# Kernel optimization log

Hardware: AMD Instinct MI355X
Metric: run time of the kernel (lower is better)

The kernel has to match this reference:

```python
import jax, jax.numpy as jnp
import numpy as np

B, IN_DIM, D, P = 256, 1024, 512, 2048


def setup_inputs() -> dict:
    key = jax.random.key(0)
    ks = jax.random.split(key, 7)
    return {
        "x": jax.random.normal(ks[0], (B, IN_DIM), dtype=jnp.float32),
        "y": jax.random.randint(ks[1], (B,), 0, P),
        "Wb": jax.random.normal(ks[2], (D, IN_DIM), dtype=jnp.float32) * 0.02,
        "bb": jax.random.normal(ks[3], (D,), dtype=jnp.float32) * 0.02,
        "Wm": jax.random.normal(ks[4], (P, D), dtype=jnp.float32) * 0.02,
        "bm": jax.random.normal(ks[5], (P,), dtype=jnp.float32) * 0.02,
        "proxies": jax.random.normal(ks[6], (P, D), dtype=jnp.float32),
    }


def reference(x, y, Wb, bb, Wm, bm, proxies):
    # backbone: Linear(in_dim -> D)
    feat = x @ Wb.T + bb                         # [B, D]
    # L2-norm regularizer: mean of per-row L2 norms
    reg_e = jnp.mean(jnp.sqrt(jnp.sum(feat * feat, axis=1)))
    # multi: classification head Linear(D -> P)
    out = feat @ Wm.T + bm                       # [B, P]
    # squared euclidean distance to each proxy (broadcast diff + square + sum)
    den = jnp.sum((feat[:, None, :] - proxies[None, :, :]) ** 2, axis=2)  # [B, P]
    # cross-entropy on negated distances
    logp = jax.nn.log_softmax(-den, axis=1)      # [B, P]
    loss = -jnp.mean(jnp.take_along_axis(logp, y[:, None], axis=1))
    return out, loss, reg_e
```

## Files before the change

### kernel.cpp

```cpp
#include <hip/hip_runtime.h>
#include <hip/hip_bf16.h>
#include <math.h>

#define NB   256
#define KIN  1024
#define ND   512
#define NP   2048
#define NTOT 4096

typedef __bf16 bf16x8 __attribute__((ext_vector_type(8)));
typedef float  f32x4  __attribute__((ext_vector_type(4)));
typedef unsigned short ush8 __attribute__((ext_vector_type(8)));

#define OFF_WPB    0u
#define OFF_FEATB  4194304u
#define OFF_PN2    4456448u
#define OFF_LOGITS 4464640u
#define OFF_ROWLP  6561792u
#define OFF_ROWNM  6562816u

__device__ __forceinline__ float bf2f(unsigned short h) {
    union { unsigned u; float f; } v; v.u = ((unsigned)h) << 16; return v.f;
}

__device__ __forceinline__ ush8 pack8(float4 f0, float4 f1) {
    union { ush8 v; __hip_bfloat162 h[4]; } o;
    o.h[0] = __float22bfloat162_rn(make_float2(f0.x, f0.y));
    o.h[1] = __float22bfloat162_rn(make_float2(f0.z, f0.w));
    o.h[2] = __float22bfloat162_rn(make_float2(f1.x, f1.y));
    o.h[3] = __float22bfloat162_rn(make_float2(f1.z, f1.w));
    return o.v;
}

__global__ __launch_bounds__(256) void k_prep(
    const float* __restrict__ Wm, const float* __restrict__ prox,
    unsigned short* __restrict__ WPb, float* __restrict__ pn2)
{
    const int t = threadIdx.x, lane = t & 63, w = t >> 6;
    const int r = blockIdx.x * 4 + w;
    const float* src = (r < NP) ? (Wm + (size_t)r * ND)
                                : (prox + (size_t)(r - NP) * ND);
    float4 v0 = *(const float4*)(src + lane * 8);
    float4 v1 = *(const float4*)(src + lane * 8 + 4);
    *(ush8*)(WPb + (size_t)r * ND + lane * 8) = pack8(v0, v1);
    if (r >= NP) {
        float s = v0.x*v0.x + v0.y*v0.y + v0.z*v0.z + v0.w*v0.w
                + v1.x*v1.x + v1.y*v1.y + v1.z*v1.z + v1.w*v1.w;
#pragma unroll
        for (int off = 32; off; off >>= 1) s += __shfl_down(s, off);
        if (lane == 0) pn2[r - NP] = s;
    }
}

__global__ __launch_bounds__(256) void k_feat(
    const float* __restrict__ x, const float* __restrict__ Wb,
    const float* __restrict__ bb, unsigned short* __restrict__ featb)
{
    __shared__ unsigned short As[2][64 * 32];
    __shared__ unsigned short Bs[2][64 * 32];
    const int t = threadIdx.x, lane = t & 63, w = t >> 6;
    const int n0 = blockIdx.x * 64, m0 = blockIdx.y * 64;
    const int srow = t >> 2, sc = (t & 3) * 8;
    const float* gA = x  + (size_t)(m0 + srow) * KIN + sc;
    const float* gB = Wb + (size_t)(n0 + srow) * KIN + sc;
    float4 a0 = *(const float4*)gA, a1 = *(const float4*)(gA + 4);
    float4 b0 = *(const float4*)gB, b1 = *(const float4*)(gB + 4);
    f32x4 acc[2][2] = {};
    const int wm = (w >> 1) * 32, wn = (w & 1) * 32;
    const int arow = wm + (lane & 15), brow = wn + (lane & 15);
    const int fcol = (lane >> 4) * 8;
    for (int ks = 0; ks < KIN / 32; ++ks) {
        *(ush8*)&As[ks & 1][srow * 32 + sc] = pack8(a0, a1);
        *(ush8*)&Bs[ks & 1][srow * 32 + sc] = pack8(b0, b1);
        __syncthreads();
        if (ks + 1 < KIN / 32) {
            a0 = *(const float4*)(gA + (ks + 1) * 32);
            a1 = *(const float4*)(gA + (ks + 1) * 32 + 4);
            b0 = *(const float4*)(gB + (ks + 1) * 32);
            b1 = *(const float4*)(gB + (ks + 1) * 32 + 4);
        }
        const unsigned short* as = &As[ks & 1][0];
        const unsigned short* bs = &Bs[ks & 1][0];
        bf16x8 af0 = *(const bf16x8*)&as[(arow     ) * 32 + fcol];
        bf16x8 af1 = *(const bf16x8*)&as[(arow + 16) * 32 + fcol];
        bf16x8 bf0 = *(const bf16x8*)&bs[(brow     ) * 32 + fcol];
        bf16x8 bf1 = *(const bf16x8*)&bs[(brow + 16) * 32 + fcol];
        acc[0][0] = __builtin_amdgcn_mfma_f32_16x16x32_bf16(af0, bf0, acc[0][0], 0, 0, 0);
        acc[0][1] = __builtin_amdgcn_mfma_f32_16x16x32_bf16(af0, bf1, acc[0][1], 0, 0, 0);
        acc[1][0] = __builtin_amdgcn_mfma_f32_16x16x32_bf16(af1, bf0, acc[1][0], 0, 0, 0);
        acc[1][1] = __builtin_amdgcn_mfma_f32_16x16x32_bf16(af1, bf1, acc[1][1], 0, 0, 0);
    }
    const int q = lane >> 4, cn = lane & 15;
#pragma unroll
    for (int i = 0; i < 2; ++i)
#pragma unroll
        for (int j = 0; j < 2; ++j) {
            const int n = n0 + wn + 16 * j + cn;
            const float bias = bb[n];
#pragma unroll
            for (int r = 0; r < 4; ++r) {
                const int m = m0 + wm + 16 * i + q * 4 + r;
                featb[m * ND + n] = __hip_bfloat16_raw(__hip_bfloat16(acc[i][j][r] + bias)).x;
            }
        }
}

__global__ __launch_bounds__(256) void k_head(
    const unsigned short* __restrict__ featb, const unsigned short* __restrict__ WPb,
    const float* __restrict__ bm, const float* __restrict__ pn2,
    float* __restrict__ out, float* __restrict__ logits)
{
    __shared__ unsigned short As[2][64 * 32];
    __shared__ unsigned short Bs[2][64 * 32];
    const int t = threadIdx.x, lane = t & 63, w = t >> 6;
    const int n0 = blockIdx.x * 64;
    const int m0 = blockIdx.y * 64;
    const int srow = t >> 2, sc = (t & 3) * 8;
    const unsigned short* gA = featb + (size_t)(m0 + srow) * ND + sc;
    const unsigned short* gB = WPb   + (size_t)(n0 + srow) * ND + sc;
    ush8 va = *(const ush8*)gA, vb = *(const ush8*)gB;
    f32x4 acc[2][2] = {};
    const int wm = (w >> 1) * 32, wn = (w & 1) * 32;
    const int fr = lane & 15, fcol = (lane >> 4) * 8;
    for (int ks = 0; ks < ND / 32; ++ks) {
        *(ush8*)&As[ks & 1][srow * 32 + sc] = va;
        *(ush8*)&Bs[ks & 1][srow * 32 + sc] = vb;
        __syncthreads();
        if (ks + 1 < ND / 32) {
            va = *(const ush8*)(gA + (ks + 1) * 32);
            vb = *(const ush8*)(gB + (ks + 1) * 32);
        }
        const unsigned short* as = &As[ks & 1][0];
        const unsigned short* bs = &Bs[ks & 1][0];
        bf16x8 af0 = *(const bf16x8*)&as[(wm      + fr) * 32 + fcol];
        bf16x8 af1 = *(const bf16x8*)&as[(wm + 16 + fr) * 32 + fcol];
        bf16x8 bf0 = *(const bf16x8*)&bs[(wn      + fr) * 32 + fcol];
        bf16x8 bf1 = *(const bf16x8*)&bs[(wn + 16 + fr) * 32 + fcol];
        acc[0][0] = __builtin_amdgcn_mfma_f32_16x16x32_bf16(af0, bf0, acc[0][0], 0, 0, 0);
        acc[0][1] = __builtin_amdgcn_mfma_f32_16x16x32_bf16(af0, bf1, acc[0][1], 0, 0, 0);
        acc[1][0] = __builtin_amdgcn_mfma_f32_16x16x32_bf16(af1, bf0, acc[1][0], 0, 0, 0);
        acc[1][1] = __builtin_amdgcn_mfma_f32_16x16x32_bf16(af1, bf1, acc[1][1], 0, 0, 0);
    }
    const bool isProxy = (n0 >= NP);
    const int q = lane >> 4;
#pragma unroll
    for (int i = 0; i < 2; ++i)
#pragma unroll
        for (int j = 0; j < 2; ++j) {
            const int n = n0 + wn + 16 * j + fr;
            const float cadd = isProxy ? pn2[n - NP] : bm[n];
#pragma unroll
            for (int r = 0; r < 4; ++r) {
                const int m = m0 + wm + 16 * i + q * 4 + r;
                const float v = acc[i][j][r];
                if (isProxy) logits[m * NP + (n - NP)] = 2.0f * v - cadd;
                else         out[m * NP + n] = v + cadd;
            }
        }
}

__device__ __forceinline__ float block_reduce(float v, float* sred, int op)
{
    const int lane = threadIdx.x & 63, wave = threadIdx.x >> 6;
#pragma unroll
    for (int off = 32; off; off >>= 1) {
        float o = __shfl_down(v, off);
        v = op ? fmaxf(v, o) : (v + o);
    }
    if (lane == 0) sred[wave] = v;
    __syncthreads();
    if (threadIdx.x == 0) {
        float r = sred[0];
#pragma unroll
        for (int wv = 1; wv < 4; ++wv) r = op ? fmaxf(r, sred[wv]) : (r + sred[wv]);
        sred[0] = r;
    }
    __syncthreads();
    float r = sred[0];
    __syncthreads();
    return r;
}

__global__ __launch_bounds__(256) void k_loss(
    const unsigned short* __restrict__ featb, const float* __restrict__ logits,
    const int* __restrict__ y, float* __restrict__ rowlp, float* __restrict__ rownm)
{
    __shared__ float sred[4];
    const int b = blockIdx.x, t = threadIdx.x;

    float s = 0.f;
#pragma unroll
    for (int c = 0; c < 2; ++c) {
        float v = bf2f(featb[b * ND + t * 2 + c]); s += v * v;
    }
    float fn2 = block_reduce(s, sred, 0);

    const float* lr = logits + (size_t)b * NP;
    float lv[8], mx = -INFINITY;
#pragma unroll
    for (int j = 0; j < 8; ++j) { lv[j] = lr[t + 256 * j]; mx = fmaxf(mx, lv[j]); }
    float MX = block_reduce(mx, sred, 1);
    float es = 0.f;
#pragma unroll
    for (int j = 0; j < 8; ++j) es += __expf(lv[j] - MX);
    float SUM = block_reduce(es, sred, 0);

    if (t == 0) {
        float ly = lr[y[b]];
        rowlp[b] = ly - MX - __logf(SUM);
        rownm[b] = sqrtf(fn2);
    }
}

__global__ __launch_bounds__(256) void k_final(
    const float* __restrict__ rowlp, const float* __restrict__ rownm,
    float* __restrict__ tail)
{
    __shared__ float sred[4];
    const int t = threadIdx.x;
    float s1 = block_reduce(rowlp[t], sred, 0);
    float s2 = block_reduce(rownm[t], sred, 0);
    if (t == 0) {
        tail[0] = -s1 / (float)NB;
        tail[1] =  s2 / (float)NB;
    }
}

extern "C" void kernel_launch(void* const* d_in, const int* in_sizes, int n_in,
                              void* d_out, int out_size, void* d_ws, size_t ws_size,
                              hipStream_t stream)
{
    const float* x       = (const float*)d_in[0];
    const int*   y       = (const int*)  d_in[1];
    const float* Wb      = (const float*)d_in[2];
    const float* bb      = (const float*)d_in[3];
    const float* Wm      = (const float*)d_in[4];
    const float* bm      = (const float*)d_in[5];
    const float* proxies = (const float*)d_in[6];

    char* ws = (char*)d_ws;
    unsigned short* WPb    = (unsigned short*)(ws + OFF_WPB);
    unsigned short* featb  = (unsigned short*)(ws + OFF_FEATB);
    float*          pn2    = (float*)(ws + OFF_PN2);
    float*          logits = (float*)(ws + OFF_LOGITS);
    float*          rowlp  = (float*)(ws + OFF_ROWLP);
    float*          rownm  = (float*)(ws + OFF_ROWNM);

    float* out  = (float*)d_out;
    float* tail = out + (size_t)NB * NP;

    k_prep <<<dim3(NTOT / 4), dim3(256), 0, stream>>>(Wm, proxies, WPb, pn2);
    k_feat <<<dim3(ND / 64, NB / 64), dim3(256), 0, stream>>>(x, Wb, bb, featb);
    k_head <<<dim3(NTOT / 64, NB / 64), dim3(256), 0, stream>>>(
        featb, WPb, bm, pn2, out, logits);
    k_loss <<<dim3(NB), dim3(256), 0, stream>>>(featb, logits, y, rowlp, rownm);
    k_final<<<dim3(1), dim3(256), 0, stream>>>(rowlp, rownm, tail);
}
```

Measured before the change: 107.7 us.

## Split-K the backbone GEMM with atomic fp32 accumulation and defer bias

The backbone GEMM previously ran only 32 blocks (8x4), each looping over all of K=1024, which leaves most CUs idle. It now splits K into 8 chunks across a z grid dimension (256 blocks) and accumulates partial sums into an fp32 feature buffer with atomicAdd. That buffer is zeroed inside the prep kernel. Bias addition and bf16 conversion move into the head GEMM's A-tile staging and the loss kernel, at the cost of more atomics, double-size feature reads, and nondeterministic summation order.

```diff
diff --git a/kernel.cpp b/kernel.cpp
--- a/kernel.cpp
+++ b/kernel.cpp
@@ -13,15 +13,11 @@
 typedef unsigned short ush8 __attribute__((ext_vector_type(8)));
 
 #define OFF_WPB    0u
-#define OFF_FEATB  4194304u
-#define OFF_PN2    4456448u
-#define OFF_LOGITS 4464640u
-#define OFF_ROWLP  6561792u
-#define OFF_ROWNM  6562816u
-
-__device__ __forceinline__ float bf2f(unsigned short h) {
-    union { unsigned u; float f; } v; v.u = ((unsigned)h) << 16; return v.f;
-}
+#define OFF_FEAT32 4194304u
+#define OFF_PN2    4718592u
+#define OFF_LOGITS 4726784u
+#define OFF_ROWLP  6823936u
+#define OFF_ROWNM  6824960u
 
 __device__ __forceinline__ ush8 pack8(float4 f0, float4 f1) {
     union { ush8 v; __hip_bfloat162 h[4]; } o;
@@ -31,12 +27,17 @@
     o.h[3] = __float22bfloat162_rn(make_float2(f1.z, f1.w));
     return o.v;
 }
+__device__ __forceinline__ float4 add4(float4 a, float4 b) {
+    return make_float4(a.x + b.x, a.y + b.y, a.z + b.z, a.w + b.w);
+}
 
 __global__ __launch_bounds__(256) void k_prep(
     const float* __restrict__ Wm, const float* __restrict__ prox,
-    unsigned short* __restrict__ WPb, float* __restrict__ pn2)
+    unsigned short* __restrict__ WPb, float* __restrict__ pn2,
+    float* __restrict__ feat32)
 {
     const int t = threadIdx.x, lane = t & 63, w = t >> 6;
+    if (t < 128) feat32[blockIdx.x * 128 + t] = 0.f;
     const int r = blockIdx.x * 4 + w;
     const float* src = (r < NP) ? (Wm + (size_t)r * ND)
                                 : (prox + (size_t)(r - NP) * ND);
@@ -54,26 +55,27 @@
 
 __global__ __launch_bounds__(256) void k_feat(
     const float* __restrict__ x, const float* __restrict__ Wb,
-    const float* __restrict__ bb, unsigned short* __restrict__ featb)
+    float* __restrict__ feat32)
 {
     __shared__ unsigned short As[2][64 * 32];
     __shared__ unsigned short Bs[2][64 * 32];
     const int t = threadIdx.x, lane = t & 63, w = t >> 6;
-    const int n0 = blockIdx.x * 64, m0 = blockIdx.y * 64;
+    const int n0 = blockIdx.x * 64, m0 = blockIdx.y * 64, k0 = blockIdx.z * 128;
     const int srow = t >> 2, sc = (t & 3) * 8;
-    const float* gA = x  + (size_t)(m0 + srow) * KIN + sc;
-    const float* gB = Wb + (size_t)(n0 + srow) * KIN + sc;
+    const float* gA = x  + (size_t)(m0 + srow) * KIN + k0 + sc;
+    const float* gB = Wb + (size_t)(n0 + srow) * KIN + k0 + sc;
     float4 a0 = *(const float4*)gA, a1 = *(const float4*)(gA + 4);
     float4 b0 = *(const float4*)gB, b1 = *(const float4*)(gB + 4);
     f32x4 acc[2][2] = {};
     const int wm = (w >> 1) * 32, wn = (w & 1) * 32;
     const int arow = wm + (lane & 15), brow = wn + (lane & 15);
     const int fcol = (lane >> 4) * 8;
-    for (int ks = 0; ks < KIN / 32; ++ks) {
+#pragma unroll
+    for (int ks = 0; ks < 4; ++ks) {
         *(ush8*)&As[ks & 1][srow * 32 + sc] = pack8(a0, a1);
         *(ush8*)&Bs[ks & 1][srow * 32 + sc] = pack8(b0, b1);
         __syncthreads();
-        if (ks + 1 < KIN / 32) {
+        if (ks + 1 < 4) {
             a0 = *(const float4*)(gA + (ks + 1) * 32);
             a1 = *(const float4*)(gA + (ks + 1) * 32 + 4);
             b0 = *(const float4*)(gB + (ks + 1) * 32);
@@ -96,17 +98,17 @@
 #pragma unroll
         for (int j = 0; j < 2; ++j) {
             const int n = n0 + wn + 16 * j + cn;
-            const float bias = bb[n];
 #pragma unroll
             for (int r = 0; r < 4; ++r) {
                 const int m = m0 + wm + 16 * i + q * 4 + r;
-                featb[m * ND + n] = __hip_bfloat16_raw(__hip_bfloat16(acc[i][j][r] + bias)).x;
+                atomicAdd(&feat32[m * ND + n], acc[i][j][r]);
             }
         }
 }
 
 __global__ __launch_bounds__(256) void k_head(
-    const unsigned short* __restrict__ featb, const unsigned short* __restrict__ WPb,
+    const float* __restrict__ feat32, const float* __restrict__ bb,
+    const unsigned short* __restrict__ WPb,
     const float* __restrict__ bm, const float* __restrict__ pn2,
     float* __restrict__ out, float* __restrict__ logits)
 {
@@ -116,18 +118,23 @@
     const int n0 = blockIdx.x * 64;
     const int m0 = blockIdx.y * 64;
     const int srow = t >> 2, sc = (t & 3) * 8;
-    const unsigned short* gA = featb + (size_t)(m0 + srow) * ND + sc;
-    const unsigned short* gB = WPb   + (size_t)(n0 + srow) * ND + sc;
-    ush8 va = *(const ush8*)gA, vb = *(const ush8*)gB;
+    const float*          gA = feat32 + (size_t)(m0 + srow) * ND + sc;
+    const unsigned short* gB = WPb    + (size_t)(n0 + srow) * ND + sc;
+    float4 a0 = *(const float4*)gA, a1 = *(const float4*)(gA + 4);
+    float4 u0 = *(const float4*)(bb + sc), u1 = *(const float4*)(bb + sc + 4);
+    ush8 vb = *(const ush8*)gB;
     f32x4 acc[2][2] = {};
     const int wm = (w >> 1) * 32, wn = (w & 1) * 32;
     const int fr = lane & 15, fcol = (lane >> 4) * 8;
     for (int ks = 0; ks < ND / 32; ++ks) {
-        *(ush8*)&As[ks & 1][srow * 32 + sc] = va;
+        *(ush8*)&As[ks & 1][srow * 32 + sc] = pack8(add4(a0, u0), add4(a1, u1));
         *(ush8*)&Bs[ks & 1][srow * 32 + sc] = vb;
         __syncthreads();
         if (ks + 1 < ND / 32) {
-            va = *(const ush8*)(gA + (ks + 1) * 32);
+            a0 = *(const float4*)(gA + (ks + 1) * 32);
+            a1 = *(const float4*)(gA + (ks + 1) * 32 + 4);
+            u0 = *(const float4*)(bb + (ks + 1) * 32 + sc);
+            u1 = *(const float4*)(bb + (ks + 1) * 32 + sc + 4);
             vb = *(const ush8*)(gB + (ks + 1) * 32);
         }
         const unsigned short* as = &As[ks & 1][0];
@@ -182,18 +189,16 @@
 }
 
 __global__ __launch_bounds__(256) void k_loss(
-    const unsigned short* __restrict__ featb, const float* __restrict__ logits,
-    const int* __restrict__ y, float* __restrict__ rowlp, float* __restrict__ rownm)
+    const float* __restrict__ feat32, const float* __restrict__ bb,
+    const float* __restrict__ logits, const int* __restrict__ y,
+    float* __restrict__ rowlp, float* __restrict__ rownm)
 {
     __shared__ float sred[4];
     const int b = blockIdx.x, t = threadIdx.x;
 
-    float s = 0.f;
-#pragma unroll
-    for (int c = 0; c < 2; ++c) {
-        float v = bf2f(featb[b * ND + t * 2 + c]); s += v * v;
-    }
-    float fn2 = block_reduce(s, sred, 0);
+    float v0 = feat32[b * ND + t] + bb[t];
+    float v1 = feat32[b * ND + t + 256] + bb[t + 256];
+    float fn2 = block_reduce(v0 * v0 + v1 * v1, sred, 0);
 
     const float* lr = logits + (size_t)b * NP;
     float lv[8], mx = -INFINITY;
@@ -240,7 +245,7 @@
 
     char* ws = (char*)d_ws;
     unsigned short* WPb    = (unsigned short*)(ws + OFF_WPB);
-    unsigned short* featb  = (unsigned short*)(ws + OFF_FEATB);
+    float*          feat32 = (float*)(ws + OFF_FEAT32);
     float*          pn2    = (float*)(ws + OFF_PN2);
     float*          logits = (float*)(ws + OFF_LOGITS);
     float*          rowlp  = (float*)(ws + OFF_ROWLP);
@@ -249,10 +254,10 @@
     float* out  = (float*)d_out;
     float* tail = out + (size_t)NB * NP;
 
-    k_prep <<<dim3(NTOT / 4), dim3(256), 0, stream>>>(Wm, proxies, WPb, pn2);
-    k_feat <<<dim3(ND / 64, NB / 64), dim3(256), 0, stream>>>(x, Wb, bb, featb);
+    k_prep <<<dim3(NTOT / 4), dim3(256), 0, stream>>>(Wm, proxies, WPb, pn2, feat32);
+    k_feat <<<dim3(ND / 64, NB / 64, 8), dim3(256), 0, stream>>>(x, Wb, feat32);
     k_head <<<dim3(NTOT / 64, NB / 64), dim3(256), 0, stream>>>(
-        featb, WPb, bm, pn2, out, logits);
-    k_loss <<<dim3(NB), dim3(256), 0, stream>>>(featb, logits, y, rowlp, rownm);
+        feat32, bb, WPb, bm, pn2, out, logits);
+    k_loss <<<dim3(NB), dim3(256), 0, stream>>>(feat32, bb, logits, y, rowlp, rownm);
     k_final<<<dim3(1), dim3(256), 0, stream>>>(rowlp, rownm, tail);
 }
```

Result: faster. 97.31 us, median of 2 (-9.6%).
